# Performance work log

Measured on AMD Instinct MI355X. Metric: run time of the kernel, lower is better.

## Reference

```python
import jax, jax.numpy as jnp
import numpy as np

IN_F, OUT_F = 4096, 14336
F8_MAX = 448.0  # max magnitude of float8_e4m3fn


def setup_inputs() -> dict:
    key = jax.random.key(0)
    kx, kw, kb = jax.random.split(key, 3)
    x = jax.random.normal(kx, (2, 512, IN_F), dtype=jnp.bfloat16)
    w = jax.random.normal(kw, (OUT_F, IN_F), dtype=jnp.float32) * 0.02
    # per-tensor scale: amax / 448 (as in F8Linear.__init__)
    w_scale = (jnp.maximum(jnp.abs(w).max(), 1e-30) / F8_MAX).astype(jnp.float32)
    # quantize to fp8 e4m3; roundtrip back to float32 so the stored values are
    # exactly the fp8-representable values (float32 container keeps the bwd
    # reference's jax.vjp happy while the math is identical)
    w_f8 = jnp.clip(w / w_scale, -F8_MAX, F8_MAX).astype(jnp.float8_e4m3fn).astype(jnp.float32)
    bias = jax.random.normal(kb, (OUT_F,), dtype=jnp.float32) * 0.02
    return {"x": x, "weight_f8": w_f8, "w_scale": w_scale, "bias": bias}


def reference(x, weight_f8, w_scale, bias):
    # dequantize to activation dtype, then GEMM: y = x @ w^T + b
    w = weight_f8.astype(x.dtype) * w_scale.astype(x.dtype)   # [out, in]
    y = jnp.einsum('bsi,oi->bso', x, w) + bias.astype(x.dtype)
    return y
```

## Files before the change

kernel.cpp:

```cpp
#include <hip/hip_runtime.h>
#include <hip/hip_bf16.h>
#include <stdint.h>


#define IN_F   4096
#define OUT_F  14336
#define M_TOT  1024

#define BM 128
#define BN 128
#define BK 64
#define KTILES (IN_F / BK)

typedef __bf16  bf16x8 __attribute__((ext_vector_type(8)));
typedef __bf16  bf16x4 __attribute__((ext_vector_type(4)));
typedef float   f32x4  __attribute__((ext_vector_type(4)));

__device__ __forceinline__ void async_copy16(const void* g, void* l) {
    __builtin_amdgcn_global_load_lds(
        (const __attribute__((address_space(1))) void*)g,
        (__attribute__((address_space(3))) void*)l,
        16, 0, 0);
}

__global__ void detect_x_dtype(const uint32_t* __restrict__ xb,
                               int* __restrict__ flag) {
    __shared__ int any_low;
    if (threadIdx.x == 0) any_low = 0;
    __syncthreads();
    uint32_t bad = 0;
    for (int i = threadIdx.x; i < 1024; i += 256) bad |= (xb[i] & 0xFFFFu);
    if (bad) atomicOr(&any_low, 1);
    __syncthreads();
    if (threadIdx.x == 0) *flag = (any_low == 0) ? 1 : 0;
}

__global__ __launch_bounds__(256) void cvt_w_kernel(
    const f32x4* __restrict__ in, bf16x8* __restrict__ out) {
    const int stride = 3584 * 256;
    for (int i = blockIdx.x * 256 + threadIdx.x; i < 7340032; i += stride) {
        f32x4 a = in[2 * i];
        f32x4 b = in[2 * i + 1];
        bf16x8 o;
        o[0] = (__bf16)a[0]; o[1] = (__bf16)a[1];
        o[2] = (__bf16)a[2]; o[3] = (__bf16)a[3];
        o[4] = (__bf16)b[0]; o[5] = (__bf16)b[1];
        o[6] = (__bf16)b[2]; o[7] = (__bf16)b[3];
        out[i] = o;
    }
}

__global__ __launch_bounds__(256) void cvt_x_kernel(
    const void* __restrict__ xraw, bf16x8* __restrict__ out,
    const int* __restrict__ flag) {
    const int f32w = (*flag != 0);
    const int i = blockIdx.x * 256 + threadIdx.x;
    if (f32w) {
        const f32x4* in = (const f32x4*)xraw;
        f32x4 a = in[2 * i];
        f32x4 b = in[2 * i + 1];
        bf16x8 o;
        o[0] = (__bf16)a[0]; o[1] = (__bf16)a[1];
        o[2] = (__bf16)a[2]; o[3] = (__bf16)a[3];
        o[4] = (__bf16)b[0]; o[5] = (__bf16)b[1];
        o[6] = (__bf16)b[2]; o[7] = (__bf16)b[3];
        out[i] = o;
    } else {
        out[i] = ((const bf16x8*)xraw)[i];
    }
}

__global__ __launch_bounds__(256) void gemm_bf16(
    const __bf16* __restrict__ xb,
    const __bf16* __restrict__ wb,
    const float*  __restrict__ w_scale,
    const float*  __restrict__ bias,
    void*         __restrict__ yraw,
    const int*    __restrict__ flag_p)
{
    __shared__ __align__(16) __bf16 As[BM * BK];
    __shared__ __align__(16) __bf16 Bs[BN * BK];

    const int f32w = (*flag_p != 0);

    const int t    = threadIdx.x;
    const int lane = t & 63;
    const int wv   = t >> 6;
    const int wm   = wv >> 1;
    const int wn   = wv & 1;
    const int lidx = lane & 15;
    const int q    = lane >> 4;

    const int flat = blockIdx.x;
    const int xcd  = flat & 7;
    const int slot = flat >> 3;
    const int ni   = xcd * 14 + (slot >> 3);
    const int mi   = slot & 7;
    const int m0   = mi * BM;
    const int n0   = ni * BN;

    const float scale = w_scale[0];

    const __bf16* ga[4]; const __bf16* gb[4];
    __bf16* la[4]; __bf16* lb[4];
    #pragma unroll
    for (int i = 0; i < 4; ++i) {
        const int s   = i * 256 + t;
        const int row = s >> 3;
        const int cgl = (s & 7) ^ (row & 7);
        ga[i] = xb + (size_t)(m0 + row) * IN_F + cgl * 8;
        gb[i] = wb + (size_t)(n0 + row) * IN_F + cgl * 8;
        la[i] = As + s * 8;
        lb[i] = Bs + s * 8;
    }

    const f32x4 zero4 = {0.f, 0.f, 0.f, 0.f};
    f32x4 acc[4][4];
    #pragma unroll
    for (int i = 0; i < 4; ++i)
        #pragma unroll
        for (int j = 0; j < 4; ++j)
            acc[i][j] = zero4;

    for (int kt = 0; kt < KTILES; ++kt) {
        #pragma unroll
        for (int i = 0; i < 4; ++i) {
            async_copy16(ga[i], la[i]);
            async_copy16(gb[i], lb[i]);
            ga[i] += BK; gb[i] += BK;
        }

        __syncthreads();

        #pragma unroll
        for (int ko = 0; ko < 2; ++ko) {
            bf16x8 afr[4], bfr[4];
            #pragma unroll
            for (int mt = 0; mt < 4; ++mt) {
                const int row = wm * 64 + mt * 16 + lidx;
                const int cgp = (ko * 4 + q) ^ (row & 7);
                afr[mt] = *reinterpret_cast<const bf16x8*>(As + row * BK + cgp * 8);
            }
            #pragma unroll
            for (int nt = 0; nt < 4; ++nt) {
                const int row = wn * 64 + nt * 16 + lidx;
                const int cgp = (ko * 4 + q) ^ (row & 7);
                bfr[nt] = *reinterpret_cast<const bf16x8*>(Bs + row * BK + cgp * 8);
            }
            #pragma unroll
            for (int mt = 0; mt < 4; ++mt)
                #pragma unroll
                for (int nt = 0; nt < 4; ++nt)
                    acc[mt][nt] = __builtin_amdgcn_mfma_f32_16x16x32_bf16(
                        afr[mt], bfr[nt], acc[mt][nt], 0, 0, 0);
        }

        __syncthreads();
    }

    float bv[4];
    #pragma unroll
    for (int nt = 0; nt < 4; ++nt)
        bv[nt] = bias[n0 + wn * 64 + nt * 16 + lidx];

    if (f32w) {
        float* yf = (float*)yraw;
        #pragma unroll
        for (int mt = 0; mt < 4; ++mt)
            #pragma unroll
            for (int r = 0; r < 4; ++r) {
                const int m = m0 + wm * 64 + mt * 16 + q * 4 + r;
                float* yp = yf + (size_t)m * OUT_F + n0 + wn * 64 + lidx;
                #pragma unroll
                for (int nt = 0; nt < 4; ++nt)
                    yp[nt * 16] = acc[mt][nt][r] * scale + bv[nt];
            }
    } else {
        __bf16* yh = (__bf16*)yraw;
        #pragma unroll
        for (int mt = 0; mt < 4; ++mt)
            #pragma unroll
            for (int r = 0; r < 4; ++r) {
                const int m = m0 + wm * 64 + mt * 16 + q * 4 + r;
                __bf16* yp = yh + (size_t)m * OUT_F + n0 + wn * 64 + lidx;
                #pragma unroll
                for (int nt = 0; nt < 4; ++nt)
                    yp[nt * 16] = (__bf16)(acc[mt][nt][r] * scale + bv[nt]);
            }
    }
}

__global__ __launch_bounds__(256) void f8linear_fallback(
    const void*  __restrict__ xraw,
    const float* __restrict__ wq,
    const float* __restrict__ w_scale,
    const float* __restrict__ bias,
    void*        __restrict__ yraw,
    const int*   __restrict__ flag_p)
{
    __shared__ __align__(16) __bf16 As[BM * 40];
    __shared__ __align__(16) __bf16 Bs[BN * 40];

    const int f32w = (*flag_p != 0);
    const int t    = threadIdx.x;
    const int lane = t & 63;
    const int wv   = t >> 6;
    const int wm   = wv >> 1;
    const int wn   = wv & 1;
    const int lidx = lane & 15;
    const int q    = lane >> 4;

    const int flat = blockIdx.x;
    const int xcd  = flat & 7;
    const int slot = flat >> 3;
    const int ni   = xcd * 14 + (slot >> 3);
    const int mi   = slot & 7;
    const int m0   = mi * BM;
    const int n0   = ni * BN;

    const float scale = w_scale[0];
    const float*  xf = (const float*)xraw;
    const __bf16* xh = (const __bf16*)xraw;

    const int af_row = t >> 3;
    const int af_col = (t & 7) * 4;
    int ah_row[2], ah_cg[2];
    #pragma unroll
    for (int i = 0; i < 2; ++i) {
        const int s = i * 256 + t;
        ah_row[i] = s >> 2;
        ah_cg[i]  = s & 3;
    }
    const int b_row = t >> 3;
    const int b_col = (t & 7) * 4;

    const f32x4 zero4 = {0.f, 0.f, 0.f, 0.f};
    f32x4 acc[4][4];
    #pragma unroll
    for (int i = 0; i < 4; ++i)
        #pragma unroll
        for (int j = 0; j < 4; ++j)
            acc[i][j] = zero4;

    f32x4  aregf[4];
    bf16x8 aregh[2];
    f32x4  breg[4];
    if (f32w) {
        #pragma unroll
        for (int i = 0; i < 4; ++i)
            aregf[i] = *reinterpret_cast<const f32x4*>(
                xf + (size_t)(m0 + af_row + i * 32) * IN_F + af_col);
    } else {
        #pragma unroll
        for (int i = 0; i < 2; ++i)
            aregh[i] = *reinterpret_cast<const bf16x8*>(
                xh + (size_t)(m0 + ah_row[i]) * IN_F + ah_cg[i] * 8);
    }
    #pragma unroll
    for (int i = 0; i < 4; ++i)
        breg[i] = *reinterpret_cast<const f32x4*>(
            wq + (size_t)(n0 + i * 32 + b_row) * IN_F + b_col);

    for (int kt = 0; kt < 128; ++kt) {
        const int k0 = kt * 32;
        if (f32w) {
            #pragma unroll
            for (int i = 0; i < 4; ++i) {
                bf16x4 pk;
                pk[0] = (__bf16)aregf[i][0];
                pk[1] = (__bf16)aregf[i][1];
                pk[2] = (__bf16)aregf[i][2];
                pk[3] = (__bf16)aregf[i][3];
                *reinterpret_cast<bf16x4*>(As + (af_row + i * 32) * 40 + af_col) = pk;
            }
        } else {
            #pragma unroll
            for (int i = 0; i < 2; ++i)
                *reinterpret_cast<bf16x8*>(As + ah_row[i] * 40 + ah_cg[i] * 8) = aregh[i];
        }
        #pragma unroll
        for (int i = 0; i < 4; ++i) {
            bf16x4 pk;
            pk[0] = (__bf16)breg[i][0];
            pk[1] = (__bf16)breg[i][1];
            pk[2] = (__bf16)breg[i][2];
            pk[3] = (__bf16)breg[i][3];
            *reinterpret_cast<bf16x4*>(Bs + (i * 32 + b_row) * 40 + b_col) = pk;
        }
        __syncthreads();
        if (kt + 1 < 128) {
            const int k1 = k0 + 32;
            if (f32w) {
                #pragma unroll
                for (int i = 0; i < 4; ++i)
                    aregf[i] = *reinterpret_cast<const f32x4*>(
                        xf + (size_t)(m0 + af_row + i * 32) * IN_F + k1 + af_col);
            } else {
                #pragma unroll
                for (int i = 0; i < 2; ++i)
                    aregh[i] = *reinterpret_cast<const bf16x8*>(
                        xh + (size_t)(m0 + ah_row[i]) * IN_F + k1 + ah_cg[i] * 8);
            }
            #pragma unroll
            for (int i = 0; i < 4; ++i)
                breg[i] = *reinterpret_cast<const f32x4*>(
                    wq + (size_t)(n0 + i * 32 + b_row) * IN_F + k1 + b_col);
        }
        bf16x8 afr[4], bfr[4];
        #pragma unroll
        for (int mt = 0; mt < 4; ++mt) {
            const int row = wm * 64 + mt * 16 + lidx;
            afr[mt] = *reinterpret_cast<const bf16x8*>(As + row * 40 + q * 8);
        }
        #pragma unroll
        for (int nt = 0; nt < 4; ++nt) {
            const int row = wn * 64 + nt * 16 + lidx;
            bfr[nt] = *reinterpret_cast<const bf16x8*>(Bs + row * 40 + q * 8);
        }
        #pragma unroll
        for (int mt = 0; mt < 4; ++mt)
            #pragma unroll
            for (int nt = 0; nt < 4; ++nt)
                acc[mt][nt] = __builtin_amdgcn_mfma_f32_16x16x32_bf16(
                    afr[mt], bfr[nt], acc[mt][nt], 0, 0, 0);
        __syncthreads();
    }

    float bv[4];
    #pragma unroll
    for (int nt = 0; nt < 4; ++nt)
        bv[nt] = bias[n0 + wn * 64 + nt * 16 + lidx];

    if (f32w) {
        float* yf = (float*)yraw;
        #pragma unroll
        for (int mt = 0; mt < 4; ++mt)
            #pragma unroll
            for (int r = 0; r < 4; ++r) {
                const int m = m0 + wm * 64 + mt * 16 + q * 4 + r;
                float* yp = yf + (size_t)m * OUT_F + n0 + wn * 64 + lidx;
                #pragma unroll
                for (int nt = 0; nt < 4; ++nt)
                    yp[nt * 16] = acc[mt][nt][r] * scale + bv[nt];
            }
    } else {
        __bf16* yh = (__bf16*)yraw;
        #pragma unroll
        for (int mt = 0; mt < 4; ++mt)
            #pragma unroll
            for (int r = 0; r < 4; ++r) {
                const int m = m0 + wm * 64 + mt * 16 + q * 4 + r;
                __bf16* yp = yh + (size_t)m * OUT_F + n0 + wn * 64 + lidx;
                #pragma unroll
                for (int nt = 0; nt < 4; ++nt)
                    yp[nt * 16] = (__bf16)(acc[mt][nt][r] * scale + bv[nt]);
            }
    }
}

extern "C" void kernel_launch(void* const* d_in, const int* in_sizes, int n_in,
                              void* d_out, int out_size, void* d_ws, size_t ws_size,
                              hipStream_t stream) {
    const void* px = nullptr; const void* pw = nullptr;
    const void* ps = nullptr; const void* pb = nullptr;
    for (int i = 0; i < n_in; ++i) {
        const long sz = in_sizes[i];
        if      (sz == (long)M_TOT * IN_F) px = d_in[i];
        else if (sz == (long)OUT_F * IN_F) pw = d_in[i];
        else if (sz == 1)                  ps = d_in[i];
        else if (sz == OUT_F)              pb = d_in[i];
    }
    if (!px) px = d_in[0];
    if (!pw) pw = d_in[1];
    if (!ps) ps = d_in[2];
    if (!pb) pb = d_in[3];

    const size_t W_BYTES  = (size_t)OUT_F * IN_F * 2;
    const size_t X_OFF    = W_BYTES;
    const size_t X_BYTES  = (size_t)M_TOT * IN_F * 2;
    const size_t FLAG_OFF = X_OFF + X_BYTES;
    const int grid = (M_TOT / BM) * (OUT_F / BN);

    if (ws_size >= FLAG_OFF + 16) {
        __bf16* wbf  = (__bf16*)d_ws;
        __bf16* xbf  = (__bf16*)((char*)d_ws + X_OFF);
        int*    flag = (int*)((char*)d_ws + FLAG_OFF);

        detect_x_dtype<<<1, 256, 0, stream>>>((const uint32_t*)px, flag);
        cvt_w_kernel<<<3584, 256, 0, stream>>>((const f32x4*)pw, (bf16x8*)wbf);
        cvt_x_kernel<<<2048, 256, 0, stream>>>(px, (bf16x8*)xbf, flag);
        gemm_bf16<<<grid, 256, 0, stream>>>(
            xbf, wbf, (const float*)ps, (const float*)pb, d_out, flag);
    } else {
        int* flag = (int*)d_ws;
        detect_x_dtype<<<1, 256, 0, stream>>>((const uint32_t*)px, flag);
        f8linear_fallback<<<grid, 256, 0, stream>>>(
            px, (const float*)pw, (const float*)ps, (const float*)pb, d_out, flag);
    }
}
```

Measured before the change: 536.4 us.

## Replace 128x128 GEMM with 256x256 eight-wave double-buffered phased pipeline

Replaces the single-buffered 128x128 bf16 GEMM with a 256x256 tile kernel using 512 threads (8 waves). It double-buffers LDS in half-tiles and interleaves async global-to-LDS staging with four MFMA phases per K step, using explicit barriers, waitcnt and setprio. The goal is to hide load latency and raise operand reuse, since the old loop stalled on a full sync every tile. The cost is 128KB of LDS, higher register pressure and a grid of only 224 blocks, which may underfill the GPU's compute units.

```diff
diff --git a/kernel.cpp b/kernel.cpp
--- a/kernel.cpp
+++ b/kernel.cpp
@@ -9,8 +9,11 @@
 
 #define BM 128
 #define BN 128
-#define BK 64
-#define KTILES (IN_F / BK)
+
+#define TM 256
+#define TN 256
+#define TK 64
+#define KT8 (IN_F / TK)
 
 typedef __bf16  bf16x8 __attribute__((ext_vector_type(8)));
 typedef __bf16  bf16x4 __attribute__((ext_vector_type(4)));
@@ -70,7 +73,7 @@
     }
 }
 
-__global__ __launch_bounds__(256) void gemm_bf16(
+__global__ __launch_bounds__(512, 2) void gemm_bf16_8ph(
     const __bf16* __restrict__ xb,
     const __bf16* __restrict__ wb,
     const float*  __restrict__ w_scale,
@@ -78,114 +81,198 @@
     void*         __restrict__ yraw,
     const int*    __restrict__ flag_p)
 {
-    __shared__ __align__(16) __bf16 As[BM * BK];
-    __shared__ __align__(16) __bf16 Bs[BN * BK];
+    __shared__ __align__(16) __bf16 As[2][2][128 * TK];
+    __shared__ __align__(16) __bf16 Bs[2][2][128 * TK];
 
     const int f32w = (*flag_p != 0);
-
     const int t    = threadIdx.x;
     const int lane = t & 63;
     const int wv   = t >> 6;
-    const int wm   = wv >> 1;
-    const int wn   = wv & 1;
+    const int wm   = wv >> 2;
+    const int wn   = wv & 3;
     const int lidx = lane & 15;
     const int q    = lane >> 4;
 
     const int flat = blockIdx.x;
     const int xcd  = flat & 7;
     const int slot = flat >> 3;
-    const int ni   = xcd * 14 + (slot >> 3);
-    const int mi   = slot & 7;
-    const int m0   = mi * BM;
-    const int n0   = ni * BN;
+    const int ni   = xcd * 7 + (slot >> 2);
+    const int mi   = slot & 3;
+    const int m0   = mi * TM;
+    const int n0   = ni * TN;
 
     const float scale = w_scale[0];
 
-    const __bf16* ga[4]; const __bf16* gb[4];
-    __bf16* la[4]; __bf16* lb[4];
-    #pragma unroll
-    for (int i = 0; i < 4; ++i) {
-        const int s   = i * 256 + t;
-        const int row = s >> 3;
-        const int cgl = (s & 7) ^ (row & 7);
-        ga[i] = xb + (size_t)(m0 + row) * IN_F + cgl * 8;
-        gb[i] = wb + (size_t)(n0 + row) * IN_F + cgl * 8;
-        la[i] = As + s * 8;
-        lb[i] = Bs + s * 8;
+    const __bf16* gA = xb + (size_t)m0 * IN_F;
+    const __bf16* gB = wb + (size_t)n0 * IN_F;
+
+    int srow[2], scgl[2];
+    #pragma unroll
+    for (int i = 0; i < 2; ++i) {
+        const int s = i * 512 + t;
+        srow[i] = s >> 3;
+        scgl[i] = (s & 7) ^ (srow[i] & 7);
+    }
+
+    int aoff[4][2], boff[2][2];
+    #pragma unroll
+    for (int qm = 0; qm < 4; ++qm) {
+        const int row = qm * 32 + wm * 16 + lidx;
+        #pragma unroll
+        for (int kg = 0; kg < 2; ++kg)
+            aoff[qm][kg] = row * 128 + (((kg * 4 + q) ^ (row & 7)) * 16);
+    }
+    #pragma unroll
+    for (int qn = 0; qn < 2; ++qn) {
+        const int row = qn * 64 + wn * 16 + lidx;
+        #pragma unroll
+        for (int kg = 0; kg < 2; ++kg)
+            boff[qn][kg] = row * 128 + (((kg * 4 + q) ^ (row & 7)) * 16);
     }
 
     const f32x4 zero4 = {0.f, 0.f, 0.f, 0.f};
-    f32x4 acc[4][4];
-    #pragma unroll
-    for (int i = 0; i < 4; ++i)
+    f32x4 acc[8][4];
+    #pragma unroll
+    for (int i = 0; i < 8; ++i)
         #pragma unroll
         for (int j = 0; j < 4; ++j)
             acc[i][j] = zero4;
 
-    for (int kt = 0; kt < KTILES; ++kt) {
-        #pragma unroll
-        for (int i = 0; i < 4; ++i) {
-            async_copy16(ga[i], la[i]);
-            async_copy16(gb[i], lb[i]);
-            ga[i] += BK; gb[i] += BK;
-        }
-
-        __syncthreads();
-
-        #pragma unroll
-        for (int ko = 0; ko < 2; ++ko) {
-            bf16x8 afr[4], bfr[4];
-            #pragma unroll
-            for (int mt = 0; mt < 4; ++mt) {
-                const int row = wm * 64 + mt * 16 + lidx;
-                const int cgp = (ko * 4 + q) ^ (row & 7);
-                afr[mt] = *reinterpret_cast<const bf16x8*>(As + row * BK + cgp * 8);
-            }
-            #pragma unroll
-            for (int nt = 0; nt < 4; ++nt) {
-                const int row = wn * 64 + nt * 16 + lidx;
-                const int cgp = (ko * 4 + q) ^ (row & 7);
-                bfr[nt] = *reinterpret_cast<const bf16x8*>(Bs + row * BK + cgp * 8);
-            }
-            #pragma unroll
-            for (int mt = 0; mt < 4; ++mt)
-                #pragma unroll
-                for (int nt = 0; nt < 4; ++nt)
-                    acc[mt][nt] = __builtin_amdgcn_mfma_f32_16x16x32_bf16(
-                        afr[mt], bfr[nt], acc[mt][nt], 0, 0, 0);
-        }
-
-        __syncthreads();
-    }
+    bf16x8 areg[4][2], breg[2][2];
+
+#define STAGE_A(tile, half) do {                                              \
+    __bf16* _dst = &As[(tile) & 1][(half)][0];                                \
+    const __bf16* _src = gA + (size_t)(half) * 128 * IN_F + (tile) * TK;      \
+    async_copy16(_src + (size_t)srow[0] * IN_F + scgl[0] * 8, _dst + t * 8);  \
+    async_copy16(_src + (size_t)srow[1] * IN_F + scgl[1] * 8,                 \
+                 _dst + (512 + t) * 8);                                       \
+} while (0)
+
+#define STAGE_B(tile, half) do {                                              \
+    __bf16* _dst = &Bs[(tile) & 1][(half)][0];                                \
+    const __bf16* _src = gB + (size_t)(half) * 128 * IN_F + (tile) * TK;      \
+    async_copy16(_src + (size_t)srow[0] * IN_F + scgl[0] * 8, _dst + t * 8);  \
+    async_copy16(_src + (size_t)srow[1] * IN_F + scgl[1] * 8,                 \
+                 _dst + (512 + t) * 8);                                       \
+} while (0)
+
+#define LOAD_A(base) do {                                                     \
+    _Pragma("unroll")                                                         \
+    for (int _qm = 0; _qm < 4; ++_qm) {                                       \
+        areg[_qm][0] = *(const bf16x8*)((base) + aoff[_qm][0]);               \
+        areg[_qm][1] = *(const bf16x8*)((base) + aoff[_qm][1]);               \
+    }                                                                         \
+} while (0)
+
+#define LOAD_B(base) do {                                                     \
+    _Pragma("unroll")                                                         \
+    for (int _qn = 0; _qn < 2; ++_qn) {                                       \
+        breg[_qn][0] = *(const bf16x8*)((base) + boff[_qn][0]);               \
+        breg[_qn][1] = *(const bf16x8*)((base) + boff[_qn][1]);               \
+    }                                                                         \
+} while (0)
+
+#define MFMA16(MO, NO) do {                                                   \
+    __builtin_amdgcn_s_setprio(1);                                            \
+    _Pragma("unroll")                                                         \
+    for (int _qm = 0; _qm < 4; ++_qm)                                         \
+        _Pragma("unroll")                                                     \
+        for (int _qn = 0; _qn < 2; ++_qn) {                                   \
+            acc[(MO) + _qm][(NO) + _qn] =                                     \
+                __builtin_amdgcn_mfma_f32_16x16x32_bf16(                      \
+                    areg[_qm][0], breg[_qn][0], acc[(MO) + _qm][(NO) + _qn],  \
+                    0, 0, 0);                                                 \
+            acc[(MO) + _qm][(NO) + _qn] =                                     \
+                __builtin_amdgcn_mfma_f32_16x16x32_bf16(                      \
+                    areg[_qm][1], breg[_qn][1], acc[(MO) + _qm][(NO) + _qn],  \
+                    0, 0, 0);                                                 \
+        }                                                                     \
+    __builtin_amdgcn_s_setprio(0);                                            \
+} while (0)
+
+#define BARR() __builtin_amdgcn_s_barrier()
+#define LGKM0() do {                                                          \
+    asm volatile("s_waitcnt lgkmcnt(0)" ::: "memory");                        \
+    __builtin_amdgcn_sched_barrier(0);                                        \
+} while (0)
+
+    STAGE_A(0, 0); STAGE_B(0, 1); STAGE_B(0, 0); STAGE_A(0, 1);
+    STAGE_A(1, 0); STAGE_B(1, 1);
+    asm volatile("s_waitcnt vmcnt(4)" ::: "memory");
+    BARR();
+
+    for (int kt = 0; kt < KT8; ++kt) {
+        const char* a0 = (const char*)&As[kt & 1][0][0];
+        const char* a1 = (const char*)&As[kt & 1][1][0];
+        const char* b0 = (const char*)&Bs[kt & 1][0][0];
+        const char* b1 = (const char*)&Bs[kt & 1][1][0];
+
+        LOAD_A(a0);
+        LOAD_B(b0);
+        if (kt + 1 < KT8) STAGE_B(kt + 1, 0);
+        BARR(); LGKM0();
+        MFMA16(0, 0);
+        BARR();
+
+        LOAD_B(b1);
+        if (kt + 1 < KT8) STAGE_A(kt + 1, 1);
+        BARR(); LGKM0();
+        MFMA16(0, 2);
+        BARR();
+
+        LOAD_A(a1);
+        if (kt + 2 < KT8) STAGE_A(kt + 2, 0);
+        BARR(); LGKM0();
+        MFMA16(4, 2);
+        BARR();
+
+        LOAD_B(b0);
+        if (kt + 2 < KT8) STAGE_B(kt + 2, 1);
+        BARR(); LGKM0();
+        MFMA16(4, 0);
+        if (kt < KT8 - 2) asm volatile("s_waitcnt vmcnt(4)" ::: "memory");
+        else              asm volatile("s_waitcnt vmcnt(0)" ::: "memory");
+        BARR();
+    }
+
+#undef STAGE_A
+#undef STAGE_B
+#undef LOAD_A
+#undef LOAD_B
+#undef MFMA16
+#undef BARR
+#undef LGKM0
 
     float bv[4];
     #pragma unroll
-    for (int nt = 0; nt < 4; ++nt)
-        bv[nt] = bias[n0 + wn * 64 + nt * 16 + lidx];
+    for (int nf = 0; nf < 4; ++nf)
+        bv[nf] = bias[n0 + (nf >> 1) * 128 + (nf & 1) * 64 + wn * 16 + lidx];
 
     if (f32w) {
         float* yf = (float*)yraw;
         #pragma unroll
-        for (int mt = 0; mt < 4; ++mt)
+        for (int mf = 0; mf < 8; ++mf)
             #pragma unroll
             for (int r = 0; r < 4; ++r) {
-                const int m = m0 + wm * 64 + mt * 16 + q * 4 + r;
-                float* yp = yf + (size_t)m * OUT_F + n0 + wn * 64 + lidx;
-                #pragma unroll
-                for (int nt = 0; nt < 4; ++nt)
-                    yp[nt * 16] = acc[mt][nt][r] * scale + bv[nt];
+                const int m = m0 + (mf >> 2) * 128 + (mf & 3) * 32 + wm * 16 + q * 4 + r;
+                float* yp = yf + (size_t)m * OUT_F + n0 + wn * 16 + lidx;
+                #pragma unroll
+                for (int nf = 0; nf < 4; ++nf)
+                    yp[(nf >> 1) * 128 + (nf & 1) * 64] =
+                        acc[mf][nf][r] * scale + bv[nf];
             }
     } else {
         __bf16* yh = (__bf16*)yraw;
         #pragma unroll
-        for (int mt = 0; mt < 4; ++mt)
+        for (int mf = 0; mf < 8; ++mf)
             #pragma unroll
             for (int r = 0; r < 4; ++r) {
-                const int m = m0 + wm * 64 + mt * 16 + q * 4 + r;
-                __bf16* yp = yh + (size_t)m * OUT_F + n0 + wn * 64 + lidx;
-                #pragma unroll
-                for (int nt = 0; nt < 4; ++nt)
-                    yp[nt * 16] = (__bf16)(acc[mt][nt][r] * scale + bv[nt]);
+                const int m = m0 + (mf >> 2) * 128 + (mf & 3) * 32 + wm * 16 + q * 4 + r;
+                __bf16* yp = yh + (size_t)m * OUT_F + n0 + wn * 16 + lidx;
+                #pragma unroll
+                for (int nf = 0; nf < 4; ++nf)
+                    yp[(nf >> 1) * 128 + (nf & 1) * 64] =
+                        (__bf16)(acc[mf][nf][r] * scale + bv[nf]);
             }
     }
 }
@@ -379,20 +466,22 @@
     const size_t X_OFF    = W_BYTES;
     const size_t X_BYTES  = (size_t)M_TOT * IN_F * 2;
     const size_t FLAG_OFF = X_OFF + X_BYTES;
-    const int grid = (M_TOT / BM) * (OUT_F / BN);
 
     if (ws_size >= FLAG_OFF + 16) {
         __bf16* wbf  = (__bf16*)d_ws;
         __bf16* xbf  = (__bf16*)((char*)d_ws + X_OFF);
         int*    flag = (int*)((char*)d_ws + FLAG_OFF);
 
+        const int grid8 = (M_TOT / TM) * (OUT_F / TN);
+
         detect_x_dtype<<<1, 256, 0, stream>>>((const uint32_t*)px, flag);
         cvt_w_kernel<<<3584, 256, 0, stream>>>((const f32x4*)pw, (bf16x8*)wbf);
         cvt_x_kernel<<<2048, 256, 0, stream>>>(px, (bf16x8*)xbf, flag);
-        gemm_bf16<<<grid, 256, 0, stream>>>(
+        gemm_bf16_8ph<<<grid8, 512, 0, stream>>>(
             xbf, wbf, (const float*)ps, (const float*)pb, d_out, flag);
     } else {
         int* flag = (int*)d_ws;
+        const int grid = (M_TOT / BM) * (OUT_F / BN);
         detect_x_dtype<<<1, 256, 0, stream>>>((const uint32_t*)px, flag);
         f8linear_fallback<<<grid, 256, 0, stream>>>(
             px, (const float*)pw, (const float*)ps, (const float*)pb, d_out, flag);
```

Measured after the change: 528.3 us. Within noise of the previous version (-1.5%).

## Fuse fp32-to-bf16 weight conversion into double-buffered GEMM mainloop

Applied to the files above, without the earlier changes.

Drops the separate weight conversion kernel. The GEMM now reads fp32 weights straight from global memory into registers, converts them to bf16 and writes them to shared memory, while activations keep using async global-to-LDS copies. The K tile shrinks to 32 with double-buffered shared memory and an occupancy hint of 4 blocks per CU, so the next tile's loads overlap the current tile's MFMAs. This removes the full write and re-read of a bf16 weight copy in workspace. In exchange the GEMM reads twice as many weight bytes per tile, and since each weight tile is re-read by 8 M-blocks, the fp32 traffic may cost more than the conversion it replaces.

```diff
diff --git a/kernel.cpp b/kernel.cpp
--- a/kernel.cpp
+++ b/kernel.cpp
@@ -9,8 +9,11 @@
 
 #define BM 128
 #define BN 128
-#define BK 64
-#define KTILES (IN_F / BK)
+
+#define TM2 128
+#define TN2 128
+#define TK2 32
+#define NT2 (IN_F / TK2)
 
 typedef __bf16  bf16x8 __attribute__((ext_vector_type(8)));
 typedef __bf16  bf16x4 __attribute__((ext_vector_type(4)));
@@ -33,21 +36,6 @@
     if (bad) atomicOr(&any_low, 1);
     __syncthreads();
     if (threadIdx.x == 0) *flag = (any_low == 0) ? 1 : 0;
-}
-
-__global__ __launch_bounds__(256) void cvt_w_kernel(
-    const f32x4* __restrict__ in, bf16x8* __restrict__ out) {
-    const int stride = 3584 * 256;
-    for (int i = blockIdx.x * 256 + threadIdx.x; i < 7340032; i += stride) {
-        f32x4 a = in[2 * i];
-        f32x4 b = in[2 * i + 1];
-        bf16x8 o;
-        o[0] = (__bf16)a[0]; o[1] = (__bf16)a[1];
-        o[2] = (__bf16)a[2]; o[3] = (__bf16)a[3];
-        o[4] = (__bf16)b[0]; o[5] = (__bf16)b[1];
-        o[6] = (__bf16)b[2]; o[7] = (__bf16)b[3];
-        out[i] = o;
-    }
 }
 
 __global__ __launch_bounds__(256) void cvt_x_kernel(
@@ -70,19 +58,18 @@
     }
 }
 
-__global__ __launch_bounds__(256) void gemm_bf16(
+__global__ __launch_bounds__(256, 4) void gemm_fused_occ(
     const __bf16* __restrict__ xb,
-    const __bf16* __restrict__ wb,
+    const float*  __restrict__ wf,
     const float*  __restrict__ w_scale,
     const float*  __restrict__ bias,
     void*         __restrict__ yraw,
     const int*    __restrict__ flag_p)
 {
-    __shared__ __align__(16) __bf16 As[BM * BK];
-    __shared__ __align__(16) __bf16 Bs[BN * BK];
+    __shared__ __align__(16) __bf16 As[2][128 * TK2];
+    __shared__ __align__(16) __bf16 Bs[2][128 * TK2];
 
     const int f32w = (*flag_p != 0);
-
     const int t    = threadIdx.x;
     const int lane = t & 63;
     const int wv   = t >> 6;
@@ -96,22 +83,34 @@
     const int slot = flat >> 3;
     const int ni   = xcd * 14 + (slot >> 3);
     const int mi   = slot & 7;
-    const int m0   = mi * BM;
-    const int n0   = ni * BN;
+    const int m0   = mi * TM2;
+    const int n0   = ni * TN2;
 
     const float scale = w_scale[0];
 
-    const __bf16* ga[4]; const __bf16* gb[4];
-    __bf16* la[4]; __bf16* lb[4];
-    #pragma unroll
-    for (int i = 0; i < 4; ++i) {
-        const int s   = i * 256 + t;
-        const int row = s >> 3;
-        const int cgl = (s & 7) ^ (row & 7);
-        ga[i] = xb + (size_t)(m0 + row) * IN_F + cgl * 8;
-        gb[i] = wb + (size_t)(n0 + row) * IN_F + cgl * 8;
-        la[i] = As + s * 8;
-        lb[i] = Bs + s * 8;
+    const __bf16* gA = xb + (size_t)m0 * IN_F;
+
+    int srow[2], slg[2];
+    #pragma unroll
+    for (int i = 0; i < 2; ++i) {
+        const int s = i * 256 + t;
+        srow[i] = s >> 2;
+        slg[i]  = (s & 3) ^ ((srow[i] >> 1) & 3);
+    }
+
+    const float* gB0 = wf + (size_t)(n0 + srow[0]) * IN_F + slg[0] * 8;
+    const float* gB1 = wf + (size_t)(n0 + srow[1]) * IN_F + slg[1] * 8;
+
+    int aoff[4], boff[4];
+    #pragma unroll
+    for (int mt = 0; mt < 4; ++mt) {
+        const int r = wm * 64 + mt * 16 + lidx;
+        aoff[mt] = r * 64 + ((q ^ ((r >> 1) & 3)) * 16);
+    }
+    #pragma unroll
+    for (int nt = 0; nt < 4; ++nt) {
+        const int r = wn * 64 + nt * 16 + lidx;
+        boff[nt] = r * 64 + ((q ^ ((r >> 1) & 3)) * 16);
     }
 
     const f32x4 zero4 = {0.f, 0.f, 0.f, 0.f};
@@ -122,41 +121,92 @@
         for (int j = 0; j < 4; ++j)
             acc[i][j] = zero4;
 
-    for (int kt = 0; kt < KTILES; ++kt) {
-        #pragma unroll
-        for (int i = 0; i < 4; ++i) {
-            async_copy16(ga[i], la[i]);
-            async_copy16(gb[i], lb[i]);
-            ga[i] += BK; gb[i] += BK;
-        }
-
-        __syncthreads();
-
-        #pragma unroll
-        for (int ko = 0; ko < 2; ++ko) {
-            bf16x8 afr[4], bfr[4];
-            #pragma unroll
-            for (int mt = 0; mt < 4; ++mt) {
-                const int row = wm * 64 + mt * 16 + lidx;
-                const int cgp = (ko * 4 + q) ^ (row & 7);
-                afr[mt] = *reinterpret_cast<const bf16x8*>(As + row * BK + cgp * 8);
-            }
-            #pragma unroll
-            for (int nt = 0; nt < 4; ++nt) {
-                const int row = wn * 64 + nt * 16 + lidx;
-                const int cgp = (ko * 4 + q) ^ (row & 7);
-                bfr[nt] = *reinterpret_cast<const bf16x8*>(Bs + row * BK + cgp * 8);
-            }
-            #pragma unroll
-            for (int mt = 0; mt < 4; ++mt)
-                #pragma unroll
-                for (int nt = 0; nt < 4; ++nt)
-                    acc[mt][nt] = __builtin_amdgcn_mfma_f32_16x16x32_bf16(
-                        afr[mt], bfr[nt], acc[mt][nt], 0, 0, 0);
-        }
-
-        __syncthreads();
-    }
+    f32x4 Br[4];
+
+#define STAGE_A(kt, BI) do {                                                  \
+    __bf16* _dst = &As[(BI)][0];                                              \
+    async_copy16(gA + (size_t)srow[0] * IN_F + (kt) * TK2 + slg[0] * 8,       \
+                 _dst + t * 8);                                               \
+    async_copy16(gA + (size_t)srow[1] * IN_F + (kt) * TK2 + slg[1] * 8,       \
+                 _dst + (256 + t) * 8);                                       \
+} while (0)
+
+#define B_LOAD(kt) do {                                                       \
+    const float* _p0 = gB0 + (kt) * TK2;                                      \
+    const float* _p1 = gB1 + (kt) * TK2;                                      \
+    Br[0] = *(const f32x4*)_p0;                                               \
+    Br[1] = *(const f32x4*)(_p0 + 4);                                         \
+    Br[2] = *(const f32x4*)_p1;                                               \
+    Br[3] = *(const f32x4*)(_p1 + 4);                                         \
+} while (0)
+
+#define B_WRITE(BI) do {                                                      \
+    __bf16* _d = &Bs[(BI)][0];                                                \
+    bf16x8 _o;                                                                \
+    _o[0] = (__bf16)Br[0][0]; _o[1] = (__bf16)Br[0][1];                       \
+    _o[2] = (__bf16)Br[0][2]; _o[3] = (__bf16)Br[0][3];                       \
+    _o[4] = (__bf16)Br[1][0]; _o[5] = (__bf16)Br[1][1];                       \
+    _o[6] = (__bf16)Br[1][2]; _o[7] = (__bf16)Br[1][3];                       \
+    *(bf16x8*)(_d + (size_t)t * 8) = _o;                                      \
+    _o[0] = (__bf16)Br[2][0]; _o[1] = (__bf16)Br[2][1];                       \
+    _o[2] = (__bf16)Br[2][2]; _o[3] = (__bf16)Br[2][3];                       \
+    _o[4] = (__bf16)Br[3][0]; _o[5] = (__bf16)Br[3][1];                       \
+    _o[6] = (__bf16)Br[3][2]; _o[7] = (__bf16)Br[3][3];                       \
+    *(bf16x8*)(_d + (size_t)(256 + t) * 8) = _o;                              \
+} while (0)
+
+#define BARR()    do { __builtin_amdgcn_s_barrier();                          \
+                       asm volatile("" ::: "memory"); } while (0)
+#define LGKM0()   asm volatile("s_waitcnt lgkmcnt(0)" ::: "memory")
+#define VMCNT(n)  asm volatile("s_waitcnt vmcnt(" #n ")" ::: "memory")
+
+    B_LOAD(0);
+    STAGE_A(0, 0);
+    VMCNT(2);
+    B_WRITE(0);
+    VMCNT(0);
+    LGKM0();
+    BARR();
+
+#define TILE_BODY(kt, P, QI) do {                                             \
+    const char* _ab = (const char*)&As[(P)][0];                               \
+    const char* _bb = (const char*)&Bs[(P)][0];                               \
+    if ((kt) + 1 < NT2) {                                                     \
+        B_LOAD((kt) + 1);                                                     \
+        STAGE_A((kt) + 1, QI);                                                \
+    }                                                                         \
+    bf16x8 afr[4], bfr[4];                                                    \
+    _Pragma("unroll")                                                         \
+    for (int _mt = 0; _mt < 4; ++_mt)                                         \
+        afr[_mt] = *(const bf16x8*)(_ab + aoff[_mt]);                         \
+    _Pragma("unroll")                                                         \
+    for (int _nt = 0; _nt < 4; ++_nt)                                         \
+        bfr[_nt] = *(const bf16x8*)(_bb + boff[_nt]);                         \
+    _Pragma("unroll")                                                         \
+    for (int _mt = 0; _mt < 4; ++_mt)                                         \
+        _Pragma("unroll")                                                     \
+        for (int _nt = 0; _nt < 4; ++_nt)                                     \
+            acc[_mt][_nt] = __builtin_amdgcn_mfma_f32_16x16x32_bf16(          \
+                afr[_mt], bfr[_nt], acc[_mt][_nt], 0, 0, 0);                  \
+    VMCNT(0);                             \
+    if ((kt) + 1 < NT2) B_WRITE(QI);                                          \
+    LGKM0();                   \
+    BARR();                                                                   \
+} while (0)
+
+    for (int it = 0; it < NT2 / 2; ++it) {
+        const int kte = 2 * it;
+        TILE_BODY(kte,     0, 1);
+        TILE_BODY(kte + 1, 1, 0);
+    }
+
+#undef TILE_BODY
+#undef STAGE_A
+#undef B_LOAD
+#undef B_WRITE
+#undef BARR
+#undef LGKM0
+#undef VMCNT
 
     float bv[4];
     #pragma unroll
@@ -375,24 +425,23 @@
     if (!ps) ps = d_in[2];
     if (!pb) pb = d_in[3];
 
-    const size_t W_BYTES  = (size_t)OUT_F * IN_F * 2;
-    const size_t X_OFF    = W_BYTES;
     const size_t X_BYTES  = (size_t)M_TOT * IN_F * 2;
-    const size_t FLAG_OFF = X_OFF + X_BYTES;
-    const int grid = (M_TOT / BM) * (OUT_F / BN);
+    const size_t FLAG_OFF = X_BYTES;
 
     if (ws_size >= FLAG_OFF + 16) {
-        __bf16* wbf  = (__bf16*)d_ws;
-        __bf16* xbf  = (__bf16*)((char*)d_ws + X_OFF);
+        __bf16* xbf  = (__bf16*)d_ws;
         int*    flag = (int*)((char*)d_ws + FLAG_OFF);
 
+        const int grid16 = (M_TOT / TM2) * (OUT_F / TN2);
+
         detect_x_dtype<<<1, 256, 0, stream>>>((const uint32_t*)px, flag);
-        cvt_w_kernel<<<3584, 256, 0, stream>>>((const f32x4*)pw, (bf16x8*)wbf);
         cvt_x_kernel<<<2048, 256, 0, stream>>>(px, (bf16x8*)xbf, flag);
-        gemm_bf16<<<grid, 256, 0, stream>>>(
-            xbf, wbf, (const float*)ps, (const float*)pb, d_out, flag);
+        gemm_fused_occ<<<grid16, 256, 0, stream>>>(
+            xbf, (const float*)pw, (const float*)ps, (const float*)pb,
+            d_out, flag);
     } else {
         int* flag = (int*)d_ws;
+        const int grid = (M_TOT / BM) * (OUT_F / BN);
         detect_x_dtype<<<1, 256, 0, stream>>>((const uint32_t*)px, flag);
         f8linear_fallback<<<grid, 256, 0, stream>>>(
             px, (const float*)pw, (const float*)ps, (const float*)pb, d_out, flag);
```

Result: slower. 611.2 us (+13.9%).
